# Kernel tuning notes

Measured on AMD Instinct MI355X. Metric: run time of the kernel, lower is better.

Reference implementation:

```python
import jax, jax.numpy as jnp
import numpy as np

U, I, D = 100000, 50000, 64
ALPHA = 0.2  # tf.nn.leaky_relu default


def seg_softmax(v, seg, n):
    # sparse row-wise softmax (tf.sparse.softmax equivalent)
    m = jax.ops.segment_max(v, seg, num_segments=n)
    e = jnp.exp(v - m[seg])
    s = jax.ops.segment_sum(e, seg, num_segments=n)
    return e / (s[seg] + 1e-12)


def spmm(att, row, col, x, n):
    # sparse_dense_matmul: out[r] = sum_e att[e] * x[col[e]]
    return jax.ops.segment_sum(att[:, None] * x[col], row, num_segments=n)


def edge_logit(raw, w, b):
    # Dense(1, sigmoid) on per-edge scalar, then exp (pre sparse-softmax)
    return jnp.exp(jax.nn.sigmoid(raw * w + b))


def graph_att(x, W, b1, w2, b2):
    # Dense(1, tanh) -> Dense(1, leaky_relu) on concat embeddings [N, 2D]
    h = jnp.tanh(x @ W + b1)  # [N]
    return jax.nn.leaky_relu(h * w2 + b2, ALPHA)


def setup_inputs() -> dict:
    key = jax.random.key(0)
    ks = jax.random.split(key, 24)
    Es, Eui, Eiu, B = 800000, 1000000, 1000000, 4096
    f32 = jnp.float32
    inp = {
        'user_embedding': jax.random.normal(ks[0], (U, D), f32) * 0.01,
        'item_embedding': jax.random.normal(ks[1], (I, D), f32) * 0.01,
        'snii1': jax.random.normal(ks[2], (Es,), f32),
        'snii2': jax.random.normal(ks[3], (Es,), f32),
        'ciii1': jax.random.normal(ks[4], (Eui,), f32),
        'ciii2': jax.random.normal(ks[5], (Eui,), f32),
        'icii1': jax.random.normal(ks[6], (Eiu,), f32),
        'icii2': jax.random.normal(ks[7], (Eiu,), f32) * 0.01,
        'low_att_w': jax.random.normal(ks[8], (6,), f32),
        'low_att_b': jax.random.normal(ks[9], (6,), f32),
        'att1_W': jax.random.normal(ks[10], (8, 2 * D), f32) * 0.1,
        'att1_b': jax.random.normal(ks[11], (8,), f32) * 0.1,
        'att2_w': jax.random.normal(ks[12], (8,), f32),
        'att2_b': jax.random.normal(ks[13], (8,), f32) * 0.1,
        'sn_row': jax.random.randint(ks[14], (Es,), 0, U, jnp.int32),
        'sn_col': jax.random.randint(ks[15], (Es,), 0, U, jnp.int32),
        'ci_row': jax.random.randint(ks[16], (Eui,), 0, U, jnp.int32),
        'ci_col': jax.random.randint(ks[17], (Eui,), 0, I, jnp.int32),
        'ic_row': jax.random.randint(ks[18], (Eiu,), 0, I, jnp.int32),
        'ic_col': jax.random.randint(ks[19], (Eiu,), 0, U, jnp.int32),
        'user_idx': jax.random.randint(ks[20], (B,), 0, U, jnp.int32),
        'item_idx': jax.random.randint(ks[21], (B,), 0, I, jnp.int32),
    }
    return inp


def reference(user_embedding, item_embedding, snii1, snii2, ciii1, ciii2,
              icii1, icii2, low_att_w, low_att_b, att1_W, att1_b, att2_w, att2_b,
              sn_row, sn_col, ci_row, ci_col, ic_row, ic_col, user_idx, item_idx):
    # low-level attention-weighted adjacency matrices (sparse softmax per row)
    sn1 = seg_softmax(edge_logit(snii1, low_att_w[0], low_att_b[0]), sn_row, U)
    sn2 = seg_softmax(edge_logit(snii2, low_att_w[1], low_att_b[1]), sn_row, U)
    ci1 = seg_softmax(edge_logit(ciii1, low_att_w[2], low_att_b[2]), ci_row, U)
    ci2 = seg_softmax(edge_logit(ciii2, low_att_w[3], low_att_b[3]), ci_row, U)
    ic1 = seg_softmax(edge_logit(icii1, low_att_w[4], low_att_b[4]), ic_row, I)
    ic2 = seg_softmax(edge_logit(icii2, low_att_w[5], low_att_b[5]), ic_row, I)

    u0, i0 = user_embedding, item_embedding

    def user_layer(u, it, att_sn, att_ci, k):
        u_from_i = spmm(att_ci, ci_row, ci_col, it, U)
        u_from_u = spmm(att_sn, sn_row, sn_col, u, U)
        a_int = jnp.exp(graph_att(jnp.concatenate([u, u_from_i], 1), att1_W[k], att1_b[k], att2_w[k], att2_b[k])) + 0.7
        a_soc = jnp.exp(graph_att(jnp.concatenate([u, u_from_u], 1), att1_W[k + 1], att1_b[k + 1], att2_w[k + 1], att2_b[k + 1])) + 0.3
        s = a_int + a_soc
        return 0.5 * u + 0.5 * ((a_int / s)[:, None] * u_from_i + (a_soc / s)[:, None] * u_from_u)

    def item_layer(u, it, att_ic, k):
        i_from_u = spmm(att_ic, ic_row, ic_col, u, I)
        a_self = jnp.exp(graph_att(jnp.concatenate([it, it], 1), att1_W[k], att1_b[k], att2_w[k], att2_b[k])) + 1.0
        a_cust = jnp.exp(graph_att(jnp.concatenate([it, i_from_u], 1), att1_W[k + 1], att1_b[k + 1], att2_w[k + 1], att2_b[k + 1])) + 1.0
        s = a_self + a_cust
        return (a_self / s)[:, None] * it + (a_cust / s)[:, None] * i_from_u

    u1 = user_layer(u0, i0, sn1, ci1, 0)
    i1 = item_layer(u0, i0, ic1, 4)
    u2 = user_layer(u1, i1, sn2, ci2, 2)
    i2 = item_layer(u1, i1, ic2, 6)

    fu = jnp.concatenate([u0, u1, u2], 1)  # [U, 3D]
    fi = jnp.concatenate([i0, i1, i2], 1)  # [I, 3D]
    return jax.nn.sigmoid(jnp.sum(fu[user_idx] * fi[item_idx], axis=1))  # [B]
```

## Files before the change

kernel.cpp:

```cpp
#include <hip/hip_runtime.h>
#include <math.h>

#define DIM 64
#define NBLK_P 512
#define NTHR 1024
#define CBSZ 1024
#define CBMAX 256


typedef unsigned short ushort_t;
typedef unsigned int uint_t;
typedef unsigned char uchar_t;
typedef float v2f __attribute__((ext_vector_type(2)));

__device__ __forceinline__ ushort_t f2bf(float f) {
    uint_t u = __float_as_uint(f);
    return (ushort_t)((u + 0x7fffu + ((u >> 16) & 1u)) >> 16);
}


__device__ __forceinline__ void count_list(const int* __restrict__ rows, int EL, int base,
                                           int* h, size_t gtid, size_t GT) {
    size_t nq = ((size_t)EL + 3) >> 2;
    for (size_t q = gtid; q < nq; q += GT) {
        int e = (int)(q << 2);
        if (e + 4 <= EL) {
            int4 r4 = *(const int4*)(rows + e);
            atomicAdd(&h[(base + r4.x) >> 10], 1);
            atomicAdd(&h[(base + r4.y) >> 10], 1);
            atomicAdd(&h[(base + r4.z) >> 10], 1);
            atomicAdd(&h[(base + r4.w) >> 10], 1);
        } else {
            for (int j = e; j < EL; j++) atomicAdd(&h[(base + rows[j]) >> 10], 1);
        }
    }
}

__global__ void count_cvt_kernel(const float* __restrict__ u0, const float* __restrict__ i0,
                                 uchar_t* __restrict__ ub, uchar_t* __restrict__ ib,
                                 size_t n8u, size_t n8t,
                                 const int* __restrict__ sn_row, const int* __restrict__ ci_row,
                                 const int* __restrict__ ic_row, int* __restrict__ cnt,
                                 int Es, int Eui, int Eiu, int U, int CB) {
    __shared__ int h[CBMAX];
    int b = blockIdx.x, tid = threadIdx.x;
    size_t gtid = (size_t)b * NTHR + tid;
    const size_t GT = (size_t)NBLK_P * NTHR;

    for (size_t i = gtid; i < n8t; i += GT) {
        const float4* src; uchar_t* dst; size_t di;
        if (i < n8u) { src = (const float4*)u0; dst = ub; di = i; }
        else         { src = (const float4*)i0; dst = ib; di = i - n8u; }
        float4 a = src[2 * di], c = src[2 * di + 1];
        int lo = 0, hi = 0;
        lo = __builtin_amdgcn_cvt_pk_fp8_f32(a.x * 256.0f, a.y * 256.0f, lo, false);
        lo = __builtin_amdgcn_cvt_pk_fp8_f32(a.z * 256.0f, a.w * 256.0f, lo, true);
        hi = __builtin_amdgcn_cvt_pk_fp8_f32(c.x * 256.0f, c.y * 256.0f, hi, false);
        hi = __builtin_amdgcn_cvt_pk_fp8_f32(c.z * 256.0f, c.w * 256.0f, hi, true);
        ((uint2*)dst)[di] = make_uint2((uint_t)lo, (uint_t)hi);
    }

    if (tid < CBMAX) h[tid] = 0;
    __syncthreads();
    count_list(sn_row, Es, 0, h, gtid, GT);
    count_list(ci_row, Eui, U, h, gtid, GT);
    count_list(ic_row, Eiu, 2 * U, h, gtid, GT);
    __syncthreads();
    if (tid < CB) cnt[(size_t)b * CB + tid] = h[tid];
}


__global__ void blkscan_kernel(const int* __restrict__ cnt, int* __restrict__ blkoff,
                               int* __restrict__ total, int CB) {
    int c = blockIdx.x;
    int b = threadIdx.x;
    int v = cnt[(size_t)b * CB + c];
    int lane = b & 63, wid = b >> 6;
    int inc = v;
    #pragma unroll
    for (int off = 1; off < 64; off <<= 1) {
        int x = __shfl_up(inc, off, 64);
        if (lane >= off) inc += x;
    }
    __shared__ int ws[NBLK_P / 64];
    if (lane == 63) ws[wid] = inc;
    __syncthreads();
    int woff = 0;
    for (int j = 0; j < wid; j++) woff += ws[j];
    blkoff[(size_t)b * CB + c] = inc - v + woff;
    if (b == NBLK_P - 1) total[c] = inc + woff;
}


__device__ __forceinline__ void cb_prefix(const int* __restrict__ total, int CB,
                                          int* cs, int* wsx) {
    int t = threadIdx.x;
    int lane = t & 63, wv = t >> 6;
    int v = 0, inc = 0;
    if (t < 256) {
        v = (t < CB) ? total[t] : 0;
        inc = v;
        #pragma unroll
        for (int off = 1; off < 64; off <<= 1) {
            int x = __shfl_up(inc, off, 64);
            if (lane >= off) inc += x;
        }
        if (lane == 63) wsx[wv] = inc;
    }
    __syncthreads();
    if (t < 256) {
        int woff = 0;
        for (int j = 0; j < wv; j++) woff += wsx[j];
        if (t < CB) cs[t] = inc - v + woff;
        if (t == CB - 1) cs[CB] = inc + woff;
    }
    __syncthreads();
}


__device__ __forceinline__ void place_edge(int v, int c, float r1, float r2,
                                           float w1, float b1, float w2, float b2,
                                           int* cur, uint2* __restrict__ barr) {
    float t1 = expf(expf(1.0f / (1.0f + expf(-(r1 * w1 + b1)))));
    float t2 = expf(expf(1.0f / (1.0f + expf(-(r2 * w2 + b2)))));
    uint_t packed = (uint_t)f2bf(t1) | ((uint_t)f2bf(t2) << 16);
    int pos = atomicAdd(&cur[v >> 10], 1);
    barr[pos] = make_uint2(((uint_t)(v & 1023) << 22) | (uint_t)c, packed);
}

__device__ __forceinline__ void place_list(const int* __restrict__ rows, const int* __restrict__ cols,
                                           const float* __restrict__ x1, const float* __restrict__ x2,
                                           int EL, int base, float w1, float b1, float w2, float b2,
                                           int* cur, uint2* __restrict__ barr,
                                           size_t gtid, size_t GT) {
    size_t nq = ((size_t)EL + 3) >> 2;
    for (size_t q = gtid; q < nq; q += GT) {
        int e = (int)(q << 2);
        if (e + 4 <= EL) {
            int4 r4 = *(const int4*)(rows + e);
            int4 c4 = *(const int4*)(cols + e);
            float4 a4 = *(const float4*)(x1 + e);
            float4 b4 = *(const float4*)(x2 + e);
            place_edge(base + r4.x, c4.x, a4.x, b4.x, w1, b1, w2, b2, cur, barr);
            place_edge(base + r4.y, c4.y, a4.y, b4.y, w1, b1, w2, b2, cur, barr);
            place_edge(base + r4.z, c4.z, a4.z, b4.z, w1, b1, w2, b2, cur, barr);
            place_edge(base + r4.w, c4.w, a4.w, b4.w, w1, b1, w2, b2, cur, barr);
        } else {
            for (int j = e; j < EL; j++)
                place_edge(base + rows[j], cols[j], x1[j], x2[j], w1, b1, w2, b2, cur, barr);
        }
    }
}

__global__ void place_kernel(const int* __restrict__ sn_row, const int* __restrict__ sn_col,
                             const int* __restrict__ ci_row, const int* __restrict__ ci_col,
                             const int* __restrict__ ic_row, const int* __restrict__ ic_col,
                             const float* __restrict__ snii1, const float* __restrict__ snii2,
                             const float* __restrict__ ciii1, const float* __restrict__ ciii2,
                             const float* __restrict__ icii1, const float* __restrict__ icii2,
                             const float* __restrict__ lw, const float* __restrict__ lb,
                             const int* __restrict__ total, const int* __restrict__ blkoff,
                             uint2* __restrict__ barr,
                             int Es, int Eui, int Eiu, int U, int CB) {
    __shared__ int cs[CBMAX + 1];
    __shared__ int wsx[4];
    __shared__ int cur[CBMAX];
    int b = blockIdx.x;
    cb_prefix(total, CB, cs, wsx);
    if (threadIdx.x < CB)
        cur[threadIdx.x] = cs[threadIdx.x] + blkoff[(size_t)b * CB + threadIdx.x];
    __syncthreads();
    size_t gtid = (size_t)b * NTHR + threadIdx.x;
    const size_t GT = (size_t)NBLK_P * NTHR;
    place_list(sn_row, sn_col, snii1, snii2, Es, 0,      lw[0], lb[0], lw[1], lb[1], cur, barr, gtid, GT);
    place_list(ci_row, ci_col, ciii1, ciii2, Eui, U,     lw[2], lb[2], lw[3], lb[3], cur, barr, gtid, GT);
    place_list(ic_row, ic_col, icii1, icii2, Eiu, 2 * U, lw[4], lb[4], lw[5], lb[5], cur, barr, gtid, GT);
}


__global__ void finalize_kernel(const uint2* __restrict__ barr, const int* __restrict__ total,
                                int* __restrict__ ptr, uint2* __restrict__ rec,
                                int R, int CB) {
    __shared__ int cs[CBMAX + 1];
    __shared__ int wsx[4];
    __shared__ int hist[CBSZ];
    __shared__ int cur2[CBSZ];
    __shared__ int wss[NTHR / 64];
    int c = blockIdx.x, tid = threadIdx.x;
    cb_prefix(total, CB, cs, wsx);
    int s0 = cs[c], s1 = cs[c + 1];
    hist[tid] = 0;
    __syncthreads();
    for (int e = s0 + tid; e < s1; e += NTHR)
        atomicAdd(&hist[barr[e].x >> 22], 1);
    __syncthreads();
    int v = hist[tid];
    int lane = tid & 63, wid = tid >> 6;
    int inc = v;
    #pragma unroll
    for (int off = 1; off < 64; off <<= 1) {
        int x = __shfl_up(inc, off, 64);
        if (lane >= off) inc += x;
    }
    if (lane == 63) wss[wid] = inc;
    __syncthreads();
    int woff = 0;
    for (int j = 0; j < wid; j++) woff += wss[j];
    int p0 = s0 + inc - v + woff;
    int r = c * CBSZ + tid;
    if (r < R) ptr[r] = p0;
    cur2[tid] = p0;
    if (c == CB - 1 && tid == 0) ptr[R] = cs[CB];
    __syncthreads();
    for (int e = s0 + tid; e < s1; e += NTHR) {
        uint2 q = barr[e];
        int rin = (int)(q.x >> 22);
        int pos = atomicAdd(&cur2[rin], 1);
        rec[pos] = make_uint2(q.x & 0x3FFFFFu, q.y);
    }
}


__device__ __forceinline__ float att_scalar(float dot, float b1, float w2, float b2, float addc) {
    float h = tanhf(dot + b1);
    float z = h * w2 + b2;
    float lr = z > 0.0f ? z : 0.2f * z;
    return expf(lr) + addc;
}

__device__ __forceinline__ void fp8_fma8v(v2f acc[4], uint2 v, float a) {
    v2f av = {a, a};
    acc[0] += av * __builtin_amdgcn_cvt_pk_f32_fp8((int)v.x, false);
    acc[1] += av * __builtin_amdgcn_cvt_pk_f32_fp8((int)v.x, true);
    acc[2] += av * __builtin_amdgcn_cvt_pk_f32_fp8((int)v.y, false);
    acc[3] += av * __builtin_amdgcn_cvt_pk_f32_fp8((int)v.y, true);
}

__device__ __forceinline__ float dot8_lanes(float d) {
    #pragma unroll
    for (int off = 1; off < 8; off <<= 1) d += __shfl_xor(d, off, 64);
    return d;
}

__device__ __forceinline__ void agg_row8(const uint2* __restrict__ rec, const uchar_t* __restrict__ tab,
                                         int e0, int e1, int l8, int lanebase,
                                         v2f acc[4], float& s) {
    if (e0 >= e1) return;
    int last = e1 - 1;
    int idx0 = e0 + l8;
    uint2 t0 = rec[min(idx0, last)];
    uint2 q;
    q.x = (idx0 <= last) ? t0.x : 0u;
    q.y = (idx0 <= last) ? t0.y : 0u;
    for (int base = e0; base < e1; base += 8) {
        int nidx = base + 8 + l8;
        uint2 tn = rec[min(nidx, last)];
        uint2 qn;
        qn.x = (nidx <= last) ? tn.x : 0u;
        qn.y = (nidx <= last) ? tn.y : 0u;
        s += __uint_as_float(q.y << 16);
        #pragma unroll
        for (int j = 0; j < 8; j++) {
            uint_t cx = __shfl(q.x, lanebase + j, 64);
            uint_t wy = __shfl(q.y, lanebase + j, 64);
            float a = __uint_as_float(wy << 16);
            uint2 v = ((const uint2*)(tab + (size_t)cx * DIM))[l8];
            fp8_fma8v(acc, v, a);
        }
        q = qn;
    }
}

__global__ void layer1_kernel(const uchar_t* __restrict__ ub8, const uchar_t* __restrict__ ib8,
                              const float* __restrict__ u0, const float* __restrict__ i0,
                              const int* __restrict__ ptr, const uint2* __restrict__ rec,
                              const float* __restrict__ W1, const float* __restrict__ b1v,
                              const float* __restrict__ w2v, const float* __restrict__ b2v,
                              float* __restrict__ u1, float* __restrict__ i1, int U, int I) {
    int gid = blockIdx.x * (blockDim.x >> 3) + (threadIdx.x >> 3);
    int lane = threadIdx.x & 63;
    int l8 = lane & 7;
    int lanebase = lane & 56;
    if (gid >= U + I) return;
    bool is_user = gid < U;
    int r = is_user ? gid : gid - U;

    v2f A[4]  = {{0.f, 0.f}, {0.f, 0.f}, {0.f, 0.f}, {0.f, 0.f}};
    v2f Bv[4] = {{0.f, 0.f}, {0.f, 0.f}, {0.f, 0.f}, {0.f, 0.f}};
    float s_a = 0.f, s_b = 0.f;

    if (is_user) {
        agg_row8(rec, ib8, ptr[U + r], ptr[U + r + 1], l8, lanebase, A, s_a);
        agg_row8(rec, ub8, ptr[r], ptr[r + 1], l8, lanebase, Bv, s_b);
    } else {
        agg_row8(rec, ub8, ptr[2 * U + r], ptr[2 * U + r + 1], l8, lanebase, A, s_a);
    }
    s_a = dot8_lanes(s_a);
    s_b = dot8_lanes(s_b);

    float ka = (1.0f / (s_a + 1e-12f)) * 0.00390625f;
    float kb = (1.0f / (s_b + 1e-12f)) * 0.00390625f;
    float ac[8], bc[8];
    #pragma unroll
    for (int j = 0; j < 4; j++) {
        ac[2 * j] = A[j][0] * ka;  ac[2 * j + 1] = A[j][1] * ka;
        bc[2 * j] = Bv[j][0] * kb; bc[2 * j + 1] = Bv[j][1] * kb;
    }

    const float* selfp = (is_user ? u0 : i0) + (size_t)r * DIM + 8 * l8;
    float4 s0 = *(const float4*)selfp;
    float4 s1 = *(const float4*)(selfp + 4);
    float sf[8] = {s0.x, s0.y, s0.z, s0.w, s1.x, s1.y, s1.z, s1.w};
    int k = is_user ? 0 : 4;
    const float* Wa = W1 + k * 2 * DIM;
    const float* Wb = Wa + 2 * DIM;
    float d1 = 0.f, d2 = 0.f;
    #pragma unroll
    for (int j = 0; j < 8; j++) {
        float wa0 = Wa[8 * l8 + j], wa1 = Wa[DIM + 8 * l8 + j];
        float wb0 = Wb[8 * l8 + j], wb1 = Wb[DIM + 8 * l8 + j];
        if (is_user) {
            d1 += sf[j] * wa0 + ac[j] * wa1;
            d2 += sf[j] * wb0 + bc[j] * wb1;
        } else {
            d1 += sf[j] * (wa0 + wa1);
            d2 += sf[j] * wb0 + ac[j] * wb1;
        }
    }
    d1 = dot8_lanes(d1);
    d2 = dot8_lanes(d2);

    float out8[8];
    float* op;
    if (is_user) {
        float a_int = att_scalar(d1, b1v[0], w2v[0], b2v[0], 0.7f);
        float a_soc = att_scalar(d2, b1v[1], w2v[1], b2v[1], 0.3f);
        float sg = a_int + a_soc;
        float wi = a_int / sg, ws = a_soc / sg;
        #pragma unroll
        for (int j = 0; j < 8; j++)
            out8[j] = 0.5f * sf[j] + 0.5f * (wi * ac[j] + ws * bc[j]);
        op = u1 + (size_t)r * DIM + 8 * l8;
    } else {
        float a_self = att_scalar(d1, b1v[4], w2v[4], b2v[4], 1.0f);
        float a_cust = att_scalar(d2, b1v[5], w2v[5], b2v[5], 1.0f);
        float sg = a_self + a_cust;
        float wi = a_self / sg, ws = a_cust / sg;
        #pragma unroll
        for (int j = 0; j < 8; j++)
            out8[j] = wi * sf[j] + ws * ac[j];
        op = i1 + (size_t)r * DIM + 8 * l8;
    }
    *(float4*)op = make_float4(out8[0], out8[1], out8[2], out8[3]);
    *(float4*)(op + 4) = make_float4(out8[4], out8[5], out8[6], out8[7]);
}


__global__ void l2f_kernel(const float* __restrict__ u0, const float* __restrict__ i0,
                           const float* __restrict__ u1, const float* __restrict__ i1,
                           const int* __restrict__ ptr, const uint2* __restrict__ rec,
                           const float* __restrict__ W1, const float* __restrict__ b1v,
                           const float* __restrict__ w2v, const float* __restrict__ b2v,
                           const int* __restrict__ uidx, const int* __restrict__ iidx,
                           float* __restrict__ out, int U, int B) {
    int wid = blockIdx.x * (blockDim.x >> 6) + (threadIdx.x >> 6);
    int lane = threadIdx.x & 63;
    if (wid >= B) return;
    int g = lane >> 3, l8 = lane & 7;
    int ru = uidx[wid], ri = iidx[wid];

    float aa[8] = {0, 0, 0, 0, 0, 0, 0, 0};
    float ab[8] = {0, 0, 0, 0, 0, 0, 0, 0};
    float s_a = 0.f, s_b = 0.f;
    int e0 = ptr[U + ru], e1 = ptr[U + ru + 1];
    for (int e = e0 + g; e < e1; e += 8) {
        uint2 q = rec[e];
        float a = __uint_as_float(q.y & 0xffff0000u);
        s_a += a;
        const float4* rp = (const float4*)(i1 + (size_t)q.x * DIM);
        float4 v0 = rp[2 * l8], v1 = rp[2 * l8 + 1];
        aa[0] = fmaf(a, v0.x, aa[0]); aa[1] = fmaf(a, v0.y, aa[1]);
        aa[2] = fmaf(a, v0.z, aa[2]); aa[3] = fmaf(a, v0.w, aa[3]);
        aa[4] = fmaf(a, v1.x, aa[4]); aa[5] = fmaf(a, v1.y, aa[5]);
        aa[6] = fmaf(a, v1.z, aa[6]); aa[7] = fmaf(a, v1.w, aa[7]);
    }
    e0 = ptr[ru]; e1 = ptr[ru + 1];
    for (int e = e0 + g; e < e1; e += 8) {
        uint2 q = rec[e];
        float a = __uint_as_float(q.y & 0xffff0000u);
        s_b += a;
        const float4* rp = (const float4*)(u1 + (size_t)q.x * DIM);
        float4 v0 = rp[2 * l8], v1 = rp[2 * l8 + 1];
        ab[0] = fmaf(a, v0.x, ab[0]); ab[1] = fmaf(a, v0.y, ab[1]);
        ab[2] = fmaf(a, v0.z, ab[2]); ab[3] = fmaf(a, v0.w, ab[3]);
        ab[4] = fmaf(a, v1.x, ab[4]); ab[5] = fmaf(a, v1.y, ab[5]);
        ab[6] = fmaf(a, v1.z, ab[6]); ab[7] = fmaf(a, v1.w, ab[7]);
    }
    #pragma unroll
    for (int off = 8; off < 64; off <<= 1) {
        s_a += __shfl_xor(s_a, off, 64);
        s_b += __shfl_xor(s_b, off, 64);
        #pragma unroll
        for (int j = 0; j < 8; j++) {
            aa[j] += __shfl_xor(aa[j], off, 64);
            ab[j] += __shfl_xor(ab[j], off, 64);
        }
    }
    float ka = 1.0f / (s_a + 1e-12f);
    float kb = 1.0f / (s_b + 1e-12f);
    #pragma unroll
    for (int j = 0; j < 8; j++) { aa[j] *= ka; ab[j] *= kb; }

    const float* sup = u1 + (size_t)ru * DIM + 8 * l8;
    float4 su0 = *(const float4*)sup;
    float4 su1 = *(const float4*)(sup + 4);
    float sfu[8] = {su0.x, su0.y, su0.z, su0.w, su1.x, su1.y, su1.z, su1.w};
    {
        const float* Wa = W1 + 2 * 2 * DIM;
        const float* Wb = Wa + 2 * DIM;
        float d1 = 0.f, d2 = 0.f;
        #pragma unroll
        for (int j = 0; j < 8; j++) {
            d1 += sfu[j] * Wa[8 * l8 + j] + aa[j] * Wa[DIM + 8 * l8 + j];
            d2 += sfu[j] * Wb[8 * l8 + j] + ab[j] * Wb[DIM + 8 * l8 + j];
        }
        d1 = dot8_lanes(d1);
        d2 = dot8_lanes(d2);
        float a_int = att_scalar(d1, b1v[2], w2v[2], b2v[2], 0.7f);
        float a_soc = att_scalar(d2, b1v[3], w2v[3], b2v[3], 0.3f);
        float sg = a_int + a_soc;
        float wi = a_int / sg, ws = a_soc / sg;
        #pragma unroll
        for (int j = 0; j < 8; j++)
            aa[j] = 0.5f * sfu[j] + 0.5f * (wi * aa[j] + ws * ab[j]);
    }

    float ac[8] = {0, 0, 0, 0, 0, 0, 0, 0};
    float s_c = 0.f;
    e0 = ptr[2 * U + ri]; e1 = ptr[2 * U + ri + 1];
    for (int e = e0 + g; e < e1; e += 8) {
        uint2 q = rec[e];
        float a = __uint_as_float(q.y & 0xffff0000u);
        s_c += a;
        const float4* rp = (const float4*)(u1 + (size_t)q.x * DIM);
        float4 v0 = rp[2 * l8], v1 = rp[2 * l8 + 1];
        ac[0] = fmaf(a, v0.x, ac[0]); ac[1] = fmaf(a, v0.y, ac[1]);
        ac[2] = fmaf(a, v0.z, ac[2]); ac[3] = fmaf(a, v0.w, ac[3]);
        ac[4] = fmaf(a, v1.x, ac[4]); ac[5] = fmaf(a, v1.y, ac[5]);
        ac[6] = fmaf(a, v1.z, ac[6]); ac[7] = fmaf(a, v1.w, ac[7]);
    }
    #pragma unroll
    for (int off = 8; off < 64; off <<= 1) {
        s_c += __shfl_xor(s_c, off, 64);
        #pragma unroll
        for (int j = 0; j < 8; j++) ac[j] += __shfl_xor(ac[j], off, 64);
    }
    float kc = 1.0f / (s_c + 1e-12f);
    #pragma unroll
    for (int j = 0; j < 8; j++) ac[j] *= kc;

    const float* sip = i1 + (size_t)ri * DIM + 8 * l8;
    float4 si0 = *(const float4*)sip;
    float4 si1 = *(const float4*)(sip + 4);
    float sfi[8] = {si0.x, si0.y, si0.z, si0.w, si1.x, si1.y, si1.z, si1.w};
    {
        const float* Wa = W1 + 6 * 2 * DIM;
        const float* Wb = Wa + 2 * DIM;
        float d1 = 0.f, d2 = 0.f;
        #pragma unroll
        for (int j = 0; j < 8; j++) {
            d1 += sfi[j] * (Wa[8 * l8 + j] + Wa[DIM + 8 * l8 + j]);
            d2 += sfi[j] * Wb[8 * l8 + j] + ac[j] * Wb[DIM + 8 * l8 + j];
        }
        d1 = dot8_lanes(d1);
        d2 = dot8_lanes(d2);
        float a_self = att_scalar(d1, b1v[6], w2v[6], b2v[6], 1.0f);
        float a_cust = att_scalar(d2, b1v[7], w2v[7], b2v[7], 1.0f);
        float sg = a_self + a_cust;
        float wi = a_self / sg, ws = a_cust / sg;
        #pragma unroll
        for (int j = 0; j < 8; j++)
            ac[j] = wi * sfi[j] + ws * ac[j];
    }

    float p = 0.f;
    #pragma unroll
    for (int j = 0; j < 8; j++) p += aa[j] * ac[j];
    p = dot8_lanes(p);
    float qd = u0[(size_t)ru * DIM + lane] * i0[(size_t)ri * DIM + lane]
             + u1[(size_t)ru * DIM + lane] * i1[(size_t)ri * DIM + lane];
    #pragma unroll
    for (int off = 32; off > 0; off >>= 1) qd += __shfl_xor(qd, off, 64);
    if (lane == 0) out[wid] = 1.0f / (1.0f + expf(-(p + qd)));
}


extern "C" void kernel_launch(void* const* d_in, const int* in_sizes, int n_in,
                              void* d_out, int out_size, void* d_ws, size_t ws_size,
                              hipStream_t stream) {
    const float* user_emb = (const float*)d_in[0];
    const float* item_emb = (const float*)d_in[1];
    const float* snii1 = (const float*)d_in[2];
    const float* snii2 = (const float*)d_in[3];
    const float* ciii1 = (const float*)d_in[4];
    const float* ciii2 = (const float*)d_in[5];
    const float* icii1 = (const float*)d_in[6];
    const float* icii2 = (const float*)d_in[7];
    const float* low_w = (const float*)d_in[8];
    const float* low_b = (const float*)d_in[9];
    const float* att1_W = (const float*)d_in[10];
    const float* att1_b = (const float*)d_in[11];
    const float* att2_w = (const float*)d_in[12];
    const float* att2_b = (const float*)d_in[13];
    const int* sn_row = (const int*)d_in[14];
    const int* sn_col = (const int*)d_in[15];
    const int* ci_row = (const int*)d_in[16];
    const int* ci_col = (const int*)d_in[17];
    const int* ic_row = (const int*)d_in[18];
    const int* ic_col = (const int*)d_in[19];
    const int* user_idx = (const int*)d_in[20];
    const int* item_idx = (const int*)d_in[21];
    float* out = (float*)d_out;

    const int Es  = in_sizes[2];
    const int Eui = in_sizes[4];
    const int Eiu = in_sizes[6];
    const int U = in_sizes[0] / DIM;
    const int I = in_sizes[1] / DIM;
    const int B = in_sizes[20];
    const int R = 2 * U + I;
    const int CB = (R + CBSZ - 1) / CBSZ;
    const int E = Es + Eui + Eiu;
    (void)E;

    char* wsb = (char*)d_ws;
    size_t off = 0;
    auto alloc = [&](size_t n_units) {
        off = (off + 3) & ~(size_t)3;
        void* p = wsb + off * 4; off += n_units; return p;
    };

    int* cnt    = (int*)alloc((size_t)NBLK_P * CB);
    int* blkoff = (int*)alloc((size_t)NBLK_P * CB);
    int* total  = (int*)alloc(CB);
    int* ptr    = (int*)alloc(R + 1);
    uint2* barr = (uint2*)alloc((size_t)E * 2);
    uint2* rec  = (uint2*)alloc((size_t)E * 2);
    uchar_t* ub8 = (uchar_t*)alloc((size_t)U * DIM / 4);
    uchar_t* ib8 = (uchar_t*)alloc((size_t)I * DIM / 4);
    float* u1  = (float*)alloc((size_t)U * DIM);
    float* i1  = (float*)alloc((size_t)I * DIM);
    (void)ws_size;

    size_t n8u = (size_t)U * DIM / 8, n8t = (size_t)(U + I) * DIM / 8;

    count_cvt_kernel<<<NBLK_P, NTHR, 0, stream>>>(user_emb, item_emb, ub8, ib8, n8u, n8t,
                                                  sn_row, ci_row, ic_row, cnt,
                                                  Es, Eui, Eiu, U, CB);
    blkscan_kernel<<<CB, NBLK_P, 0, stream>>>(cnt, blkoff, total, CB);
    place_kernel<<<NBLK_P, NTHR, 0, stream>>>(sn_row, sn_col, ci_row, ci_col, ic_row, ic_col,
                                              snii1, snii2, ciii1, ciii2, icii1, icii2,
                                              low_w, low_b, total, blkoff, barr,
                                              Es, Eui, Eiu, U, CB);
    finalize_kernel<<<CB, NTHR, 0, stream>>>(barr, total, ptr, rec, R, CB);

    layer1_kernel<<<(U + I + 31) / 32, 256, 0, stream>>>(ub8, ib8, user_emb, item_emb,
        ptr, rec, att1_W, att1_b, att2_w, att2_b, u1, i1, U, I);

    l2f_kernel<<<(B + 3) / 4, 256, 0, stream>>>(user_emb, item_emb, u1, i1, ptr, rec,
        att1_W, att1_b, att2_w, att2_b, user_idx, item_idx, out, U, B);
}
```

Before: 290.6 us.

## Fuse graph build kernels into one cooperative kernel with grid syncs

Merges the count/convert, block scan, placement and per-bucket finalize kernels into a single cooperative kernel that uses grid-wide syncs between phases. It also halves the persistent block count to 256. This aims to remove several launch gaps and redundant prefix recomputation. In exchange it adds grid barrier costs and less parallelism, and finalize now only covers buckets with index below the block count, which could miss buckets if CB exceeds 256.

```diff
diff --git a/kernel.cpp b/kernel.cpp
--- a/kernel.cpp
+++ b/kernel.cpp
@@ -1,8 +1,11 @@
 #include <hip/hip_runtime.h>
+#include <hip/hip_cooperative_groups.h>
 #include <math.h>
 
+namespace cg = cooperative_groups;
+
 #define DIM 64
-#define NBLK_P 512
+#define NBLK_C 256
 #define NTHR 1024
 #define CBSZ 1024
 #define CBMAX 256
@@ -35,88 +38,6 @@
         }
     }
 }
-
-__global__ void count_cvt_kernel(const float* __restrict__ u0, const float* __restrict__ i0,
-                                 uchar_t* __restrict__ ub, uchar_t* __restrict__ ib,
-                                 size_t n8u, size_t n8t,
-                                 const int* __restrict__ sn_row, const int* __restrict__ ci_row,
-                                 const int* __restrict__ ic_row, int* __restrict__ cnt,
-                                 int Es, int Eui, int Eiu, int U, int CB) {
-    __shared__ int h[CBMAX];
-    int b = blockIdx.x, tid = threadIdx.x;
-    size_t gtid = (size_t)b * NTHR + tid;
-    const size_t GT = (size_t)NBLK_P * NTHR;
-
-    for (size_t i = gtid; i < n8t; i += GT) {
-        const float4* src; uchar_t* dst; size_t di;
-        if (i < n8u) { src = (const float4*)u0; dst = ub; di = i; }
-        else         { src = (const float4*)i0; dst = ib; di = i - n8u; }
-        float4 a = src[2 * di], c = src[2 * di + 1];
-        int lo = 0, hi = 0;
-        lo = __builtin_amdgcn_cvt_pk_fp8_f32(a.x * 256.0f, a.y * 256.0f, lo, false);
-        lo = __builtin_amdgcn_cvt_pk_fp8_f32(a.z * 256.0f, a.w * 256.0f, lo, true);
-        hi = __builtin_amdgcn_cvt_pk_fp8_f32(c.x * 256.0f, c.y * 256.0f, hi, false);
-        hi = __builtin_amdgcn_cvt_pk_fp8_f32(c.z * 256.0f, c.w * 256.0f, hi, true);
-        ((uint2*)dst)[di] = make_uint2((uint_t)lo, (uint_t)hi);
-    }
-
-    if (tid < CBMAX) h[tid] = 0;
-    __syncthreads();
-    count_list(sn_row, Es, 0, h, gtid, GT);
-    count_list(ci_row, Eui, U, h, gtid, GT);
-    count_list(ic_row, Eiu, 2 * U, h, gtid, GT);
-    __syncthreads();
-    if (tid < CB) cnt[(size_t)b * CB + tid] = h[tid];
-}
-
-
-__global__ void blkscan_kernel(const int* __restrict__ cnt, int* __restrict__ blkoff,
-                               int* __restrict__ total, int CB) {
-    int c = blockIdx.x;
-    int b = threadIdx.x;
-    int v = cnt[(size_t)b * CB + c];
-    int lane = b & 63, wid = b >> 6;
-    int inc = v;
-    #pragma unroll
-    for (int off = 1; off < 64; off <<= 1) {
-        int x = __shfl_up(inc, off, 64);
-        if (lane >= off) inc += x;
-    }
-    __shared__ int ws[NBLK_P / 64];
-    if (lane == 63) ws[wid] = inc;
-    __syncthreads();
-    int woff = 0;
-    for (int j = 0; j < wid; j++) woff += ws[j];
-    blkoff[(size_t)b * CB + c] = inc - v + woff;
-    if (b == NBLK_P - 1) total[c] = inc + woff;
-}
-
-
-__device__ __forceinline__ void cb_prefix(const int* __restrict__ total, int CB,
-                                          int* cs, int* wsx) {
-    int t = threadIdx.x;
-    int lane = t & 63, wv = t >> 6;
-    int v = 0, inc = 0;
-    if (t < 256) {
-        v = (t < CB) ? total[t] : 0;
-        inc = v;
-        #pragma unroll
-        for (int off = 1; off < 64; off <<= 1) {
-            int x = __shfl_up(inc, off, 64);
-            if (lane >= off) inc += x;
-        }
-        if (lane == 63) wsx[wv] = inc;
-    }
-    __syncthreads();
-    if (t < 256) {
-        int woff = 0;
-        for (int j = 0; j < wv; j++) woff += wsx[j];
-        if (t < CB) cs[t] = inc - v + woff;
-        if (t == CB - 1) cs[CB] = inc + woff;
-    }
-    __syncthreads();
-}
-
 
 __device__ __forceinline__ void place_edge(int v, int c, float r1, float r2,
                                            float w1, float b1, float w2, float b2,
@@ -152,71 +73,139 @@
     }
 }
 
-__global__ void place_kernel(const int* __restrict__ sn_row, const int* __restrict__ sn_col,
-                             const int* __restrict__ ci_row, const int* __restrict__ ci_col,
-                             const int* __restrict__ ic_row, const int* __restrict__ ic_col,
-                             const float* __restrict__ snii1, const float* __restrict__ snii2,
-                             const float* __restrict__ ciii1, const float* __restrict__ ciii2,
-                             const float* __restrict__ icii1, const float* __restrict__ icii2,
-                             const float* __restrict__ lw, const float* __restrict__ lb,
-                             const int* __restrict__ total, const int* __restrict__ blkoff,
-                             uint2* __restrict__ barr,
-                             int Es, int Eui, int Eiu, int U, int CB) {
+
+__global__ __launch_bounds__(NTHR, 4)
+void build_kernel(const float* __restrict__ u0f, const float* __restrict__ i0f,
+                  uchar_t* __restrict__ ub, uchar_t* __restrict__ ib,
+                  size_t n8u, size_t n8t,
+                  const int* __restrict__ sn_row, const int* __restrict__ sn_col,
+                  const int* __restrict__ ci_row, const int* __restrict__ ci_col,
+                  const int* __restrict__ ic_row, const int* __restrict__ ic_col,
+                  const float* __restrict__ snii1, const float* __restrict__ snii2,
+                  const float* __restrict__ ciii1, const float* __restrict__ ciii2,
+                  const float* __restrict__ icii1, const float* __restrict__ icii2,
+                  const float* __restrict__ lw, const float* __restrict__ lb,
+                  int* __restrict__ cnt, int* __restrict__ blkoff, int* __restrict__ total,
+                  int* __restrict__ ptr, uint2* __restrict__ barr, uint2* __restrict__ rec,
+                  int Es, int Eui, int Eiu, int U, int R, int CB) {
+    cg::grid_group grid = cg::this_grid();
+    __shared__ int h[CBMAX];
+    __shared__ int ws2[4];
     __shared__ int cs[CBMAX + 1];
     __shared__ int wsx[4];
     __shared__ int cur[CBMAX];
-    int b = blockIdx.x;
-    cb_prefix(total, CB, cs, wsx);
-    if (threadIdx.x < CB)
-        cur[threadIdx.x] = cs[threadIdx.x] + blkoff[(size_t)b * CB + threadIdx.x];
+    __shared__ int hist[CBSZ];
+    __shared__ int cur2[CBSZ];
+    __shared__ int wss[NTHR / 64];
+
+    int b = blockIdx.x, tid = threadIdx.x;
+    size_t gtid = (size_t)b * NTHR + tid;
+    const size_t GT = (size_t)NBLK_C * NTHR;
+
+    for (size_t i = gtid; i < n8t; i += GT) {
+        const float4* src; uchar_t* dst; size_t di;
+        if (i < n8u) { src = (const float4*)u0f; dst = ub; di = i; }
+        else         { src = (const float4*)i0f; dst = ib; di = i - n8u; }
+        float4 a = src[2 * di], c = src[2 * di + 1];
+        int lo = 0, hi = 0;
+        lo = __builtin_amdgcn_cvt_pk_fp8_f32(a.x * 256.0f, a.y * 256.0f, lo, false);
+        lo = __builtin_amdgcn_cvt_pk_fp8_f32(a.z * 256.0f, a.w * 256.0f, lo, true);
+        hi = __builtin_amdgcn_cvt_pk_fp8_f32(c.x * 256.0f, c.y * 256.0f, hi, false);
+        hi = __builtin_amdgcn_cvt_pk_fp8_f32(c.z * 256.0f, c.w * 256.0f, hi, true);
+        ((uint2*)dst)[di] = make_uint2((uint_t)lo, (uint_t)hi);
+    }
+    if (tid < CBMAX) h[tid] = 0;
     __syncthreads();
-    size_t gtid = (size_t)b * NTHR + threadIdx.x;
-    const size_t GT = (size_t)NBLK_P * NTHR;
+    count_list(sn_row, Es, 0, h, gtid, GT);
+    count_list(ci_row, Eui, U, h, gtid, GT);
+    count_list(ic_row, Eiu, 2 * U, h, gtid, GT);
+    __syncthreads();
+    if (tid < CB) cnt[(size_t)b * CB + tid] = h[tid];
+    grid.sync();
+
+    if (b < CB) {
+        int lane = tid & 63, wv = tid >> 6;
+        int v = 0, inc = 0;
+        if (tid < NBLK_C) {
+            v = cnt[(size_t)tid * CB + b];
+            inc = v;
+            #pragma unroll
+            for (int off = 1; off < 64; off <<= 1) {
+                int x = __shfl_up(inc, off, 64);
+                if (lane >= off) inc += x;
+            }
+            if (lane == 63) ws2[wv] = inc;
+        }
+        __syncthreads();
+        if (tid < NBLK_C) {
+            int woff = 0;
+            for (int j = 0; j < wv; j++) woff += ws2[j];
+            blkoff[(size_t)tid * CB + b] = inc - v + woff;
+            if (tid == NBLK_C - 1) total[b] = inc + woff;
+        }
+    }
+    grid.sync();
+
+    {
+        int lane = tid & 63, wv = tid >> 6;
+        int v = 0, inc = 0;
+        if (tid < 256) {
+            v = (tid < CB) ? total[tid] : 0;
+            inc = v;
+            #pragma unroll
+            for (int off = 1; off < 64; off <<= 1) {
+                int x = __shfl_up(inc, off, 64);
+                if (lane >= off) inc += x;
+            }
+            if (lane == 63) wsx[wv] = inc;
+        }
+        __syncthreads();
+        if (tid < 256) {
+            int woff = 0;
+            for (int j = 0; j < wv; j++) woff += wsx[j];
+            if (tid < CB) cs[tid] = inc - v + woff;
+            if (tid == CB - 1) cs[CB] = inc + woff;
+        }
+        __syncthreads();
+    }
+    if (tid < CB) cur[tid] = cs[tid] + blkoff[(size_t)b * CB + tid];
+    __syncthreads();
     place_list(sn_row, sn_col, snii1, snii2, Es, 0,      lw[0], lb[0], lw[1], lb[1], cur, barr, gtid, GT);
     place_list(ci_row, ci_col, ciii1, ciii2, Eui, U,     lw[2], lb[2], lw[3], lb[3], cur, barr, gtid, GT);
     place_list(ic_row, ic_col, icii1, icii2, Eiu, 2 * U, lw[4], lb[4], lw[5], lb[5], cur, barr, gtid, GT);
-}
-
-
-__global__ void finalize_kernel(const uint2* __restrict__ barr, const int* __restrict__ total,
-                                int* __restrict__ ptr, uint2* __restrict__ rec,
-                                int R, int CB) {
-    __shared__ int cs[CBMAX + 1];
-    __shared__ int wsx[4];
-    __shared__ int hist[CBSZ];
-    __shared__ int cur2[CBSZ];
-    __shared__ int wss[NTHR / 64];
-    int c = blockIdx.x, tid = threadIdx.x;
-    cb_prefix(total, CB, cs, wsx);
-    int s0 = cs[c], s1 = cs[c + 1];
-    hist[tid] = 0;
-    __syncthreads();
-    for (int e = s0 + tid; e < s1; e += NTHR)
-        atomicAdd(&hist[barr[e].x >> 22], 1);
-    __syncthreads();
-    int v = hist[tid];
-    int lane = tid & 63, wid = tid >> 6;
-    int inc = v;
-    #pragma unroll
-    for (int off = 1; off < 64; off <<= 1) {
-        int x = __shfl_up(inc, off, 64);
-        if (lane >= off) inc += x;
-    }
-    if (lane == 63) wss[wid] = inc;
-    __syncthreads();
-    int woff = 0;
-    for (int j = 0; j < wid; j++) woff += wss[j];
-    int p0 = s0 + inc - v + woff;
-    int r = c * CBSZ + tid;
-    if (r < R) ptr[r] = p0;
-    cur2[tid] = p0;
-    if (c == CB - 1 && tid == 0) ptr[R] = cs[CB];
-    __syncthreads();
-    for (int e = s0 + tid; e < s1; e += NTHR) {
-        uint2 q = barr[e];
-        int rin = (int)(q.x >> 22);
-        int pos = atomicAdd(&cur2[rin], 1);
-        rec[pos] = make_uint2(q.x & 0x3FFFFFu, q.y);
+    grid.sync();
+
+    if (b < CB) {
+        int s0 = cs[b], s1 = cs[b + 1];
+        hist[tid] = 0;
+        __syncthreads();
+        for (int e = s0 + tid; e < s1; e += NTHR)
+            atomicAdd(&hist[barr[e].x >> 22], 1);
+        __syncthreads();
+        int v = hist[tid];
+        int lane = tid & 63, wv = tid >> 6;
+        int inc = v;
+        #pragma unroll
+        for (int off = 1; off < 64; off <<= 1) {
+            int x = __shfl_up(inc, off, 64);
+            if (lane >= off) inc += x;
+        }
+        if (lane == 63) wss[wv] = inc;
+        __syncthreads();
+        int woff = 0;
+        for (int j = 0; j < wv; j++) woff += wss[j];
+        int p0 = s0 + inc - v + woff;
+        int r = b * CBSZ + tid;
+        if (r < R) ptr[r] = p0;
+        cur2[tid] = p0;
+        if (b == CB - 1 && tid == 0) ptr[R] = cs[CB];
+        __syncthreads();
+        for (int e = s0 + tid; e < s1; e += NTHR) {
+            uint2 q = barr[e];
+            int rin = (int)(q.x >> 22);
+            int pos = atomicAdd(&cur2[rin], 1);
+            rec[pos] = make_uint2(q.x & 0x3FFFFFu, q.y);
+        }
     }
 }
 
@@ -540,8 +529,8 @@
         void* p = wsb + off * 4; off += n_units; return p;
     };
 
-    int* cnt    = (int*)alloc((size_t)NBLK_P * CB);
-    int* blkoff = (int*)alloc((size_t)NBLK_P * CB);
+    int* cnt    = (int*)alloc((size_t)NBLK_C * CB);
+    int* blkoff = (int*)alloc((size_t)NBLK_C * CB);
     int* total  = (int*)alloc(CB);
     int* ptr    = (int*)alloc(R + 1);
     uint2* barr = (uint2*)alloc((size_t)E * 2);
@@ -554,15 +543,20 @@
 
     size_t n8u = (size_t)U * DIM / 8, n8t = (size_t)(U + I) * DIM / 8;
 
-    count_cvt_kernel<<<NBLK_P, NTHR, 0, stream>>>(user_emb, item_emb, ub8, ib8, n8u, n8t,
-                                                  sn_row, ci_row, ic_row, cnt,
-                                                  Es, Eui, Eiu, U, CB);
-    blkscan_kernel<<<CB, NBLK_P, 0, stream>>>(cnt, blkoff, total, CB);
-    place_kernel<<<NBLK_P, NTHR, 0, stream>>>(sn_row, sn_col, ci_row, ci_col, ic_row, ic_col,
-                                              snii1, snii2, ciii1, ciii2, icii1, icii2,
-                                              low_w, low_b, total, blkoff, barr,
-                                              Es, Eui, Eiu, U, CB);
-    finalize_kernel<<<CB, NTHR, 0, stream>>>(barr, total, ptr, rec, R, CB);
+    int Es_ = Es, Eui_ = Eui, Eiu_ = Eiu, U_ = U, R_ = R, CB_ = CB;
+    void* kargs[] = {
+        (void*)&user_emb, (void*)&item_emb, (void*)&ub8, (void*)&ib8,
+        (void*)&n8u, (void*)&n8t,
+        (void*)&sn_row, (void*)&sn_col, (void*)&ci_row, (void*)&ci_col,
+        (void*)&ic_row, (void*)&ic_col,
+        (void*)&snii1, (void*)&snii2, (void*)&ciii1, (void*)&ciii2,
+        (void*)&icii1, (void*)&icii2, (void*)&low_w, (void*)&low_b,
+        (void*)&cnt, (void*)&blkoff, (void*)&total, (void*)&ptr,
+        (void*)&barr, (void*)&rec,
+        (void*)&Es_, (void*)&Eui_, (void*)&Eiu_, (void*)&U_, (void*)&R_, (void*)&CB_
+    };
+    hipLaunchCooperativeKernel((void*)build_kernel, dim3(NBLK_C), dim3(NTHR),
+                               kargs, 0, stream);
 
     layer1_kernel<<<(U + I + 31) / 32, 256, 0, stream>>>(ub8, ib8, user_emb, item_emb,
         ptr, rec, att1_W, att1_b, att2_w, att2_b, u1, i1, U, I);
```

Result: slower. 418.2 us (+43.9%).
